# Kernel optimization log

Measured on AMD Instinct MI355X. Metric: run time of the kernel, lower is better.

The kernel has to match this reference:

```python
import jax, jax.numpy as jnp
import numpy as np

N_NODES = 50000
N_EDGES = 800000
IN_CH = 128
HID = 64
HEADS = 4
OUT_CH = 32
NEG_SLOPE = 0.2


def _glorot(key, shape):
    fan = shape[0] + shape[-1]
    return jax.random.normal(key, shape, dtype=jnp.float32) * jnp.sqrt(2.0 / fan)


def setup_inputs() -> dict:
    key = jax.random.key(0)
    ks = jax.random.split(key, 10)
    x = jax.random.normal(ks[0], (N_NODES, IN_CH), dtype=jnp.float32)
    edge_index = jax.random.randint(ks[1], (2, N_EDGES), 0, N_NODES, dtype=jnp.int32)
    # Layer 1: in -> HEADS*HID, concat=True
    W1 = _glorot(ks[2], (IN_CH, HEADS * HID))
    att_src1 = _glorot(ks[3], (HEADS, HID))
    att_dst1 = _glorot(ks[4], (HEADS, HID))
    b1 = jnp.zeros((HEADS * HID,), dtype=jnp.float32)
    # Layer 2: HEADS*HID -> OUT_CH, heads=1, concat=False
    W2 = _glorot(ks[5], (HEADS * HID, OUT_CH))
    att_src2 = _glorot(ks[6], (1, OUT_CH))
    att_dst2 = _glorot(ks[7], (1, OUT_CH))
    b2 = jnp.zeros((OUT_CH,), dtype=jnp.float32)
    return {"x": x, "edge_index": edge_index, "W1": W1, "att_src1": att_src1,
            "att_dst1": att_dst1, "b1": b1, "W2": W2, "att_src2": att_src2,
            "att_dst2": att_dst2, "b2": b2}


def _segment_softmax(logits, seg, num_segments):
    # logits: [E, H], softmax over edges sharing the same target node
    m = jax.ops.segment_max(logits, seg, num_segments=num_segments)  # [N, H]
    ex = jnp.exp(logits - m[seg])
    s = jax.ops.segment_sum(ex, seg, num_segments=num_segments)
    return ex / (s[seg] + 1e-16)


def _gat_layer(x, edge_index, W, att_src, att_dst, bias, heads, concat):
    N = x.shape[0]
    C = att_src.shape[-1]
    h = (x @ W).reshape(N, heads, C)                 # [N, H, C]
    a_src = jnp.sum(h * att_src, axis=-1)            # [N, H]
    a_dst = jnp.sum(h * att_dst, axis=-1)            # [N, H]
    src, dst = edge_index[0], edge_index[1]
    logits = jax.nn.leaky_relu(a_src[src] + a_dst[dst], NEG_SLOPE)  # [E, H]
    alpha = _segment_softmax(logits, dst, N)         # [E, H]
    msg = h[src] * alpha[:, :, None]                 # [E, H, C]
    out = jax.ops.segment_sum(msg, dst, num_segments=N)  # [N, H, C]
    out = out.reshape(N, heads * C) if concat else out.mean(axis=1)
    return out + bias


def reference(x, edge_index, W1, att_src1, att_dst1, b1, W2, att_src2, att_dst2, b2):
    # dropout omitted (eval mode)
    h = _gat_layer(x, edge_index, W1, att_src1, att_dst1, b1, HEADS, True)
    h = jax.nn.elu(h)
    out = _gat_layer(h, edge_index, W2, att_src2, att_dst2, b2, 1, False)
    return out
```

## Files before the change

kernel.cpp:

```cpp
#include <hip/hip_runtime.h>
#include <hip/hip_bf16.h>
#include <hip/hip_fp16.h>

#define NEG_SLOPE 0.2f

typedef _Float16 half8 __attribute__((ext_vector_type(8)));
typedef float f32x4 __attribute__((ext_vector_type(4)));

__device__ __forceinline__ float lrelu(float x) { return x >= 0.f ? x : NEG_SLOPE * x; }

__device__ __forceinline__ float4 h4_to_f4(float2 r) {
    __half2 a = *(__half2*)&r.x;
    __half2 b = *(__half2*)&r.y;
    float2 fa = __half22float2(a), fb = __half22float2(b);
    return make_float4(fa.x, fa.y, fb.x, fb.y);
}

__device__ __forceinline__ void fma4(float a, float4 v, float4& acc) {
    acc.x = fmaf(a, v.x, acc.x); acc.y = fmaf(a, v.y, acc.y);
    acc.z = fmaf(a, v.z, acc.z); acc.w = fmaf(a, v.w, acc.w);
}


__global__ void k_hist(const int* __restrict__ dst, int* __restrict__ counts, int E) {
    int e = blockIdx.x * 256 + threadIdx.x;
    if (e < E) atomicAdd(&counts[dst[e]], 1);
}

__global__ __launch_bounds__(256) void k_scan1(const int* __restrict__ counts,
                                               int* __restrict__ bsum, int N) {
    __shared__ int wsum[4];
    int b = blockIdx.x, t = threadIdx.x;
    int i0 = b * 1024 + t * 4;
    int s = 0;
    if (i0 < N) { int4 v = *(const int4*)&counts[i0]; s = v.x + v.y + v.z + v.w; }
#pragma unroll
    for (int off = 32; off; off >>= 1) s += __shfl_down(s, off);
    if ((t & 63) == 0) wsum[t >> 6] = s;
    __syncthreads();
    if (t == 0) bsum[b] = wsum[0] + wsum[1] + wsum[2] + wsum[3];
}

__global__ void k_scan2(const int* __restrict__ bsum, int* __restrict__ boff,
                        int* __restrict__ row_ptrN, int nb) {
    int t = threadIdx.x;
    int v = (t < nb) ? bsum[t] : 0;
    int incl = v;
#pragma unroll
    for (int off = 1; off < 64; off <<= 1) {
        int u = __shfl_up(incl, off);
        if (t >= off) incl += u;
    }
    if (t < nb) boff[t] = incl - v;
    if (t == nb - 1) *row_ptrN = incl;
}

__global__ __launch_bounds__(256) void k_scan3(const int* __restrict__ counts,
                                               const int* __restrict__ boff,
                                               int* __restrict__ row_ptr,
                                               int* __restrict__ row_fill, int N) {
    __shared__ int lds[256];
    int b = blockIdx.x, t = threadIdx.x;
    int i0 = b * 1024 + t * 4;
    int4 v = make_int4(0, 0, 0, 0);
    if (i0 < N) v = *(const int4*)&counts[i0];
    int tot = v.x + v.y + v.z + v.w;
    lds[t] = tot;
    __syncthreads();
    for (int off = 1; off < 256; off <<= 1) {
        int u = (t >= off) ? lds[t - off] : 0;
        __syncthreads();
        lds[t] += u;
        __syncthreads();
    }
    int excl = lds[t] - tot;
    int run = boff[b] + excl;
    if (i0 < N) {
        row_ptr[i0] = run;     row_fill[i0] = run;     run += v.x;
        row_ptr[i0 + 1] = run; row_fill[i0 + 1] = run; run += v.y;
        row_ptr[i0 + 2] = run; row_fill[i0 + 2] = run; run += v.z;
        row_ptr[i0 + 3] = run; row_fill[i0 + 3] = run;
    }
}

__global__ void k_scatter(const int* __restrict__ src, const int* __restrict__ dst,
                          int* __restrict__ row_fill, int* __restrict__ esrc, int E) {
    int e = blockIdx.x * 256 + threadIdx.x;
    if (e < E) {
        int p = atomicAdd(&row_fill[dst[e]], 1);
        esrc[p] = src[e];
    }
}


__global__ __launch_bounds__(128) void k_w1t(const float* __restrict__ W,
                                             __half* __restrict__ Wt) {
    int n = blockIdx.x;
    int k = threadIdx.x;
    Wt[n * 128 + k] = __float2half(W[(size_t)k * 256 + n]);
}


__global__ __launch_bounds__(256, 3) void k_gemm1(const float* __restrict__ x,
                                                  const __half* __restrict__ Wt,
                                                  const float* __restrict__ att_src,
                                                  const float* __restrict__ att_dst,
                                                  __half* __restrict__ h,
                                                  float* __restrict__ a_s,
                                                  float* __restrict__ a_d, int M) {
    __shared__ __align__(16) __half Xs[64 * 128];
    __shared__ __align__(16) __half Ws[128 * 128];
    const int tid = threadIdx.x;
    const int row0 = blockIdx.x * 64;
    const int by = blockIdx.y;
    const int col0 = by * 128;

    for (int t = 0; t < 4; ++t) {
        int c = tid + t * 256;
        int row = c >> 4, ch = c & 15;
        int r = row0 + row;
        float4 va = make_float4(0.f, 0.f, 0.f, 0.f), vb = va;
        if (r < M) {
            va = *(const float4*)&x[(size_t)r * 128 + ch * 8];
            vb = *(const float4*)&x[(size_t)r * 128 + ch * 8 + 4];
        }
        half8 hv;
        hv[0] = (_Float16)va.x; hv[1] = (_Float16)va.y;
        hv[2] = (_Float16)va.z; hv[3] = (_Float16)va.w;
        hv[4] = (_Float16)vb.x; hv[5] = (_Float16)vb.y;
        hv[6] = (_Float16)vb.z; hv[7] = (_Float16)vb.w;
        *(half8*)((char*)Xs + row * 256 + ((ch * 16) ^ ((row & 7) << 4))) = hv;
    }
    for (int t = 0; t < 8; ++t) {
        int c = tid + t * 256;
        int n = c >> 4, ch = c & 15;
        float4 v = *(const float4*)&Wt[(size_t)(col0 + n) * 128 + ch * 8];
        *(float4*)((char*)Ws + n * 256 + ((ch * 16) ^ ((n & 7) << 4))) = v;
    }
    __syncthreads();

    const int w = tid >> 6, lane = tid & 63;
    const int col_l = lane & 15, kgrp = lane >> 4;
    const int arow = w * 16 + col_l;
    const int sw = (col_l & 7) << 4;

    f32x4 acc[8];
#pragma unroll
    for (int nt = 0; nt < 8; ++nt) acc[nt] = (f32x4){0.f, 0.f, 0.f, 0.f};

#pragma unroll
    for (int ks = 0; ks < 4; ++ks) {
        int kchunk = (ks * 4 + kgrp) * 16;
        half8 av = *(const half8*)((const char*)Xs + arow * 256 + (kchunk ^ sw));
#pragma unroll
        for (int nt = 0; nt < 8; ++nt) {
            half8 bv = *(const half8*)((const char*)Ws + (nt * 16 + col_l) * 256 + (kchunk ^ sw));
            acc[nt] = __builtin_amdgcn_mfma_f32_16x16x32_f16(av, bv, acc[nt], 0, 0, 0);
        }
    }

    float asv[8], adv[8];
#pragma unroll
    for (int nt = 0; nt < 8; ++nt) {
        int gc = col0 + nt * 16 + col_l;
        asv[nt] = att_src[gc];
        adv[nt] = att_dst[gc];
    }
    const int rbase = row0 + w * 16 + kgrp * 4;
#pragma unroll
    for (int reg = 0; reg < 4; ++reg) {
        int gr = rbase + reg;
        if (gr < M) {
#pragma unroll
            for (int nt = 0; nt < 8; ++nt)
                h[(size_t)gr * 256 + col0 + nt * 16 + col_l] = __float2half(acc[nt][reg]);
        }
        float s0 = 0.f, d0 = 0.f, s1 = 0.f, d1 = 0.f;
#pragma unroll
        for (int nt = 0; nt < 4; ++nt) {
            s0 = fmaf(acc[nt][reg], asv[nt], s0);
            d0 = fmaf(acc[nt][reg], adv[nt], d0);
            s1 = fmaf(acc[nt + 4][reg], asv[nt + 4], s1);
            d1 = fmaf(acc[nt + 4][reg], adv[nt + 4], d1);
        }
#pragma unroll
        for (int off = 1; off < 16; off <<= 1) {
            s0 += __shfl_xor(s0, off); d0 += __shfl_xor(d0, off);
            s1 += __shfl_xor(s1, off); d1 += __shfl_xor(d1, off);
        }
        if (col_l == 0 && gr < M) {
            a_s[(size_t)gr * 4 + by * 2]     = s0;
            a_s[(size_t)gr * 4 + by * 2 + 1] = s1;
            a_d[(size_t)gr * 4 + by * 2]     = d0;
            a_d[(size_t)gr * 4 + by * 2 + 1] = d1;
        }
    }
}


__global__ __launch_bounds__(256) void k_alpha1(const float* __restrict__ asrc,
                                                const float* __restrict__ adst,
                                                const int* __restrict__ row_ptr,
                                                const int* __restrict__ esrc,
                                                float* __restrict__ alpha, int N) {
    int wv = threadIdx.x >> 6, lane = threadIdx.x & 63;
    int n = blockIdx.x * 4 + wv;
    if (n >= N) return;
    int e0 = row_ptr[n], e1 = row_ptr[n + 1];
    int deg = e1 - e0;
    if (deg == 0) return;
    const float4 ad = *(const float4*)&adst[(size_t)n * 4];
    if (deg <= 64) {
        float4 l = make_float4(-3e38f, -3e38f, -3e38f, -3e38f);
        if (lane < deg) {
            int s = esrc[e0 + lane];
            float4 as = *(const float4*)&asrc[(size_t)s * 4];
            l.x = lrelu(as.x + ad.x); l.y = lrelu(as.y + ad.y);
            l.z = lrelu(as.z + ad.z); l.w = lrelu(as.w + ad.w);
        }
        float4 m = l;
#pragma unroll
        for (int off = 32; off; off >>= 1) {
            m.x = fmaxf(m.x, __shfl_xor(m.x, off));
            m.y = fmaxf(m.y, __shfl_xor(m.y, off));
            m.z = fmaxf(m.z, __shfl_xor(m.z, off));
            m.w = fmaxf(m.w, __shfl_xor(m.w, off));
        }
        if (lane < deg) {
            float4 p;
            p.x = __expf(l.x - m.x); p.y = __expf(l.y - m.y);
            p.z = __expf(l.z - m.z); p.w = __expf(l.w - m.w);
            *(float4*)&alpha[(size_t)(e0 + lane) * 4] = p;
        }
    } else {
        float4 m = make_float4(-3e38f, -3e38f, -3e38f, -3e38f);
        for (int p0 = e0; p0 < e1; p0 += 64) {
            int e = p0 + lane;
            if (e < e1) {
                int s = esrc[e];
                float4 as = *(const float4*)&asrc[(size_t)s * 4];
                m.x = fmaxf(m.x, lrelu(as.x + ad.x));
                m.y = fmaxf(m.y, lrelu(as.y + ad.y));
                m.z = fmaxf(m.z, lrelu(as.z + ad.z));
                m.w = fmaxf(m.w, lrelu(as.w + ad.w));
            }
        }
#pragma unroll
        for (int off = 32; off; off >>= 1) {
            m.x = fmaxf(m.x, __shfl_xor(m.x, off));
            m.y = fmaxf(m.y, __shfl_xor(m.y, off));
            m.z = fmaxf(m.z, __shfl_xor(m.z, off));
            m.w = fmaxf(m.w, __shfl_xor(m.w, off));
        }
        for (int p0 = e0; p0 < e1; p0 += 64) {
            int e = p0 + lane;
            if (e < e1) {
                int s = esrc[e];
                float4 as = *(const float4*)&asrc[(size_t)s * 4];
                float4 p;
                p.x = __expf(lrelu(as.x + ad.x) - m.x);
                p.y = __expf(lrelu(as.y + ad.y) - m.y);
                p.z = __expf(lrelu(as.z + ad.z) - m.z);
                p.w = __expf(lrelu(as.w + ad.w) - m.w);
                *(float4*)&alpha[(size_t)e * 4] = p;
            }
        }
    }
}


__global__ __launch_bounds__(256) void k_agg1(const __half* __restrict__ h1,
                                              const int* __restrict__ row_ptr,
                                              const int* __restrict__ esrc,
                                              const float* __restrict__ alpha,
                                              const float* __restrict__ b1,
                                              float* __restrict__ y1, int N) {
    __shared__ int ss[4][64];
    __shared__ float sa[4][64 * 4];
    int tid = threadIdx.x;
    int wv = tid >> 6, lane = tid & 63;
    int n = blockIdx.x * 4 + wv;
    if (n >= N) return;
    int head = lane >> 4;
    int e0 = row_ptr[n], e1 = row_ptr[n + 1];
    float4 acc = make_float4(0.f, 0.f, 0.f, 0.f);
    float4 asum = make_float4(0.f, 0.f, 0.f, 0.f);

    for (int p0 = e0; p0 < e1; p0 += 64) {
        int cnt = min(64, e1 - p0);
        if (lane < cnt) {
            ss[wv][lane] = esrc[p0 + lane];
            float4 a4 = *(const float4*)&alpha[(size_t)(p0 + lane) * 4];
            *(float4*)&sa[wv][lane * 4] = a4;
            asum.x += a4.x; asum.y += a4.y; asum.z += a4.z; asum.w += a4.w;
        }
        int i = 0;
        for (; i + 3 < cnt; i += 4) {
            int s0 = ss[wv][i], s1 = ss[wv][i + 1], s2 = ss[wv][i + 2], s3 = ss[wv][i + 3];
            float a0 = sa[wv][i * 4 + head],       a1 = sa[wv][(i + 1) * 4 + head];
            float a2 = sa[wv][(i + 2) * 4 + head], a3 = sa[wv][(i + 3) * 4 + head];
            float2 r0 = *(const float2*)&h1[(size_t)s0 * 256 + lane * 4];
            float2 r1 = *(const float2*)&h1[(size_t)s1 * 256 + lane * 4];
            float2 r2 = *(const float2*)&h1[(size_t)s2 * 256 + lane * 4];
            float2 r3 = *(const float2*)&h1[(size_t)s3 * 256 + lane * 4];
            fma4(a0, h4_to_f4(r0), acc);
            fma4(a1, h4_to_f4(r1), acc);
            fma4(a2, h4_to_f4(r2), acc);
            fma4(a3, h4_to_f4(r3), acc);
        }
        for (; i < cnt; ++i) {
            int s0 = ss[wv][i];
            float a0 = sa[wv][i * 4 + head];
            float2 r0 = *(const float2*)&h1[(size_t)s0 * 256 + lane * 4];
            fma4(a0, h4_to_f4(r0), acc);
        }
    }

#pragma unroll
    for (int off = 1; off < 64; off <<= 1) {
        asum.x += __shfl_xor(asum.x, off);
        asum.y += __shfl_xor(asum.y, off);
        asum.z += __shfl_xor(asum.z, off);
        asum.w += __shfl_xor(asum.w, off);
    }
    float ssum = (head == 0) ? asum.x : (head == 1) ? asum.y : (head == 2) ? asum.z : asum.w;
    float inv = 1.f / (ssum + 1e-16f);
    float4 bb = *(const float4*)&b1[lane * 4];
    float4 v;
    v.x = acc.x * inv + bb.x; v.y = acc.y * inv + bb.y;
    v.z = acc.z * inv + bb.z; v.w = acc.w * inv + bb.w;
    v.x = (v.x > 0.f) ? v.x : (__expf(v.x) - 1.f);
    v.y = (v.y > 0.f) ? v.y : (__expf(v.y) - 1.f);
    v.z = (v.z > 0.f) ? v.z : (__expf(v.z) - 1.f);
    v.w = (v.w > 0.f) ? v.w : (__expf(v.w) - 1.f);
    *(float4*)&y1[(size_t)n * 256 + lane * 4] = v;
}


__global__ __launch_bounds__(256) void k_gemm2(const float* __restrict__ y1,
                                               const float* __restrict__ W,
                                               const float* __restrict__ att_src,
                                               const float* __restrict__ att_dst,
                                               __half* __restrict__ h2,
                                               float* __restrict__ a_s,
                                               float* __restrict__ a_d, int M) {
    __shared__ float xs[256][32];
    __shared__ float ws2[256 * 32];
    int tid = threadIdx.x;
    int row0 = blockIdx.x * 32;
    for (int t = tid; t < 2048; t += 256) {
        int k4 = t >> 5, m = t & 31;
        int r = row0 + m;
        float4 v = make_float4(0.f, 0.f, 0.f, 0.f);
        if (r < M) v = *(const float4*)&y1[(size_t)r * 256 + k4 * 4];
        xs[k4 * 4 + 0][m] = v.x;
        xs[k4 * 4 + 1][m] = v.y;
        xs[k4 * 4 + 2][m] = v.z;
        xs[k4 * 4 + 3][m] = v.w;
    }
    for (int t = tid; t < 2048; t += 256)
        *(float4*)&ws2[t * 4] = *(const float4*)&W[t * 4];
    __syncthreads();

    int tx = tid & 7, ty = tid >> 3;
    float acc[4] = {};
#pragma unroll 4
    for (int k = 0; k < 256; ++k) {
        float a = xs[k][ty];
        float4 b = *(const float4*)&ws2[k * 32 + tx * 4];
        acc[0] += a * b.x; acc[1] += a * b.y; acc[2] += a * b.z; acc[3] += a * b.w;
    }
    int r = row0 + ty;
    if (r < M) {
        __half2 p01 = __floats2half2_rn(acc[0], acc[1]);
        __half2 p23 = __floats2half2_rn(acc[2], acc[3]);
        float2 st;
        *(__half2*)&st.x = p01;
        *(__half2*)&st.y = p23;
        *(float2*)&h2[(size_t)r * 32 + tx * 4] = st;
    }

    float s_ = 0.f, d_ = 0.f;
#pragma unroll
    for (int j = 0; j < 4; ++j) {
        s_ = fmaf(acc[j], att_src[tx * 4 + j], s_);
        d_ = fmaf(acc[j], att_dst[tx * 4 + j], d_);
    }
#pragma unroll
    for (int off = 1; off < 8; off <<= 1) {
        s_ += __shfl_xor(s_, off);
        d_ += __shfl_xor(d_, off);
    }
    if (tx == 0 && r < M) { a_s[r] = s_; a_d[r] = d_; }
}


__global__ __launch_bounds__(256) void k_alpha2(const float* __restrict__ asrc,
                                                const float* __restrict__ adst,
                                                const int* __restrict__ row_ptr,
                                                const int* __restrict__ esrc,
                                                float* __restrict__ alpha, int N) {
    int g = threadIdx.x >> 5, c = threadIdx.x & 31;
    int n = blockIdx.x * 8 + g;
    if (n >= N) return;
    int e0 = row_ptr[n], e1 = row_ptr[n + 1];
    int deg = e1 - e0;
    if (deg == 0) return;
    float ad = adst[n];
    if (deg <= 32) {
        float l = -3e38f;
        if (c < deg) l = lrelu(asrc[esrc[e0 + c]] + ad);
        float m = l;
#pragma unroll
        for (int off = 16; off; off >>= 1) m = fmaxf(m, __shfl_xor(m, off, 32));
        if (c < deg) alpha[e0 + c] = __expf(l - m);
    } else {
        float m = -3e38f;
        for (int p0 = e0; p0 < e1; p0 += 32) {
            int e = p0 + c;
            if (e < e1) m = fmaxf(m, lrelu(asrc[esrc[e]] + ad));
        }
#pragma unroll
        for (int off = 16; off; off >>= 1) m = fmaxf(m, __shfl_xor(m, off, 32));
        for (int p0 = e0; p0 < e1; p0 += 32) {
            int e = p0 + c;
            if (e < e1) alpha[e] = __expf(lrelu(asrc[esrc[e]] + ad) - m);
        }
    }
}


__global__ __launch_bounds__(256) void k_agg2(const __half* __restrict__ h2,
                                              const int* __restrict__ row_ptr,
                                              const int* __restrict__ esrc,
                                              const float* __restrict__ alpha,
                                              const float* __restrict__ b2,
                                              float* __restrict__ out, int N) {
    __shared__ int ss[4][64];
    __shared__ float sa[4][64];
    int tid = threadIdx.x;
    int wv = tid >> 6, lane = tid & 63;
    int n = blockIdx.x * 4 + wv;
    if (n >= N) return;
    int grp = lane >> 4, cl = lane & 15;
    int e0 = row_ptr[n], e1 = row_ptr[n + 1];
    float2 acc = make_float2(0.f, 0.f);
    float asum = 0.f;

    for (int p0 = e0; p0 < e1; p0 += 64) {
        int cnt = min(64, e1 - p0);
        if (lane < cnt) {
            ss[wv][lane] = esrc[p0 + lane];
            float a = alpha[p0 + lane];
            sa[wv][lane] = a;
            asum += a;
        }
        int i = 0;
        for (; i + 7 < cnt; i += 8) {
            int ea = i + grp, eb = i + 4 + grp;
            int s0 = ss[wv][ea], s1 = ss[wv][eb];
            float a0 = sa[wv][ea], a1 = sa[wv][eb];
            __half2 v0 = *(const __half2*)&h2[(size_t)s0 * 32 + cl * 2];
            __half2 v1 = *(const __half2*)&h2[(size_t)s1 * 32 + cl * 2];
            float2 f0 = __half22float2(v0), f1 = __half22float2(v1);
            acc.x = fmaf(a0, f0.x, acc.x); acc.y = fmaf(a0, f0.y, acc.y);
            acc.x = fmaf(a1, f1.x, acc.x); acc.y = fmaf(a1, f1.y, acc.y);
        }
        for (; i < cnt; i += 4) {
            int e = i + grp;
            if (e < cnt) {
                int s0 = ss[wv][e];
                float a0 = sa[wv][e];
                __half2 v0 = *(const __half2*)&h2[(size_t)s0 * 32 + cl * 2];
                float2 f0 = __half22float2(v0);
                acc.x = fmaf(a0, f0.x, acc.x); acc.y = fmaf(a0, f0.y, acc.y);
            }
        }
    }
    acc.x += __shfl_xor(acc.x, 16); acc.y += __shfl_xor(acc.y, 16);
    acc.x += __shfl_xor(acc.x, 32); acc.y += __shfl_xor(acc.y, 32);
#pragma unroll
    for (int off = 1; off < 64; off <<= 1) asum += __shfl_xor(asum, off);
    if (grp == 0) {
        float inv = 1.f / (asum + 1e-16f);
        float2 o;
        o.x = acc.x * inv + b2[cl * 2];
        o.y = acc.y * inv + b2[cl * 2 + 1];
        *(float2*)&out[(size_t)n * 32 + cl * 2] = o;
    }
}


extern "C" void kernel_launch(void* const* d_in, const int* in_sizes, int n_in,
                              void* d_out, int out_size, void* d_ws, size_t ws_size,
                              hipStream_t stream) {
    const float* x   = (const float*)d_in[0];
    const int*   ei  = (const int*)d_in[1];
    const float* W1  = (const float*)d_in[2];
    const float* as1 = (const float*)d_in[3];
    const float* ad1 = (const float*)d_in[4];
    const float* b1  = (const float*)d_in[5];
    const float* W2  = (const float*)d_in[6];
    const float* as2 = (const float*)d_in[7];
    const float* ad2 = (const float*)d_in[8];
    const float* b2  = (const float*)d_in[9];
    float* out = (float*)d_out;

    const int N = in_sizes[0] / 128;
    const int E = in_sizes[1] / 2;
    const int* src = ei;
    const int* dstp = ei + E;
    const int nb = (N + 1023) / 1024;

    char* ws = (char*)d_ws;
    size_t off = 0;
    auto alloc = [&](size_t nbytes) {
        void* p = ws + off;
        off += (nbytes + 255) & ~(size_t)255;
        return p;
    };
    int* counts    = (int*)alloc((size_t)N * 4);
    int* row_ptr   = (int*)alloc((size_t)(N + 1) * 4);
    int* row_fill  = (int*)alloc((size_t)N * 4);
    int* esrc      = (int*)alloc((size_t)E * 4);
    __half* h1     = (__half*)alloc((size_t)N * 256 * 2);
    float* y1      = (float*)alloc((size_t)N * 256 * 4);
    __half* h2     = (__half*)alloc((size_t)N * 32 * 2);
    float* a_s1    = (float*)alloc((size_t)N * 4 * 4);
    float* a_d1    = (float*)alloc((size_t)N * 4 * 4);
    float* a_s2    = (float*)alloc((size_t)N * 4);
    float* a_d2    = (float*)alloc((size_t)N * 4);
    float* alpha1  = (float*)alloc((size_t)E * 4 * 4);
    float* alpha2  = (float*)alloc((size_t)E * 4);
    int* bsum      = (int*)alloc((size_t)nb * 4);
    int* boff      = (int*)alloc((size_t)nb * 4);
    __half* Wt     = (__half*)alloc((size_t)256 * 128 * 2);

    hipMemsetAsync(counts, 0, (size_t)N * 4, stream);
    k_hist<<<(E + 255) / 256, 256, 0, stream>>>(dstp, counts, E);
    k_scan1<<<nb, 256, 0, stream>>>(counts, bsum, N);
    k_scan2<<<1, 64, 0, stream>>>(bsum, boff, &row_ptr[N], nb);
    k_scan3<<<nb, 256, 0, stream>>>(counts, boff, row_ptr, row_fill, N);
    k_scatter<<<(E + 255) / 256, 256, 0, stream>>>(src, dstp, row_fill, esrc, E);

    k_w1t<<<256, 128, 0, stream>>>(W1, Wt);
    k_gemm1<<<dim3((N + 63) / 64, 2), 256, 0, stream>>>(x, Wt, as1, ad1, h1, a_s1, a_d1, N);
    k_alpha1<<<(N + 3) / 4, 256, 0, stream>>>(a_s1, a_d1, row_ptr, esrc, alpha1, N);
    k_agg1<<<(N + 3) / 4, 256, 0, stream>>>(h1, row_ptr, esrc, alpha1, b1, y1, N);

    k_gemm2<<<(N + 31) / 32, 256, 0, stream>>>(y1, W2, as2, ad2, h2, a_s2, a_d2, N);
    k_alpha2<<<(N + 7) / 8, 256, 0, stream>>>(a_s2, a_d2, row_ptr, esrc, alpha2, N);
    k_agg2<<<(N + 3) / 4, 256, 0, stream>>>(h2, row_ptr, esrc, alpha2, b2, out, N);
}
```

Measured before the change: 267.2 us.

## Fuse edge-softmax into aggregation kernels and run layer-2 GEMM on fp16 MFMA

```diff
diff --git a/kernel.cpp b/kernel.cpp
--- a/kernel.cpp
+++ b/kernel.cpp
@@ -100,6 +100,13 @@
     Wt[n * 128 + k] = __float2half(W[(size_t)k * 256 + n]);
 }
 
+__global__ __launch_bounds__(256) void k_w2t(const float* __restrict__ W,
+                                             __half* __restrict__ Wt) {
+    int n = blockIdx.x;
+    int k = threadIdx.x;
+    Wt[n * 256 + k] = __float2half(W[(size_t)k * 32 + n]);
+}
+
 
 __global__ __launch_bounds__(256, 3) void k_gemm1(const float* __restrict__ x,
                                                   const __half* __restrict__ Wt,
@@ -198,39 +205,69 @@
 }
 
 
-__global__ __launch_bounds__(256) void k_alpha1(const float* __restrict__ asrc,
-                                                const float* __restrict__ adst,
-                                                const int* __restrict__ row_ptr,
-                                                const int* __restrict__ esrc,
-                                                float* __restrict__ alpha, int N) {
-    int wv = threadIdx.x >> 6, lane = threadIdx.x & 63;
+__global__ __launch_bounds__(256) void k_agg1(const __half* __restrict__ h1,
+                                              const int* __restrict__ row_ptr,
+                                              const int* __restrict__ esrc,
+                                              const float* __restrict__ asrc,
+                                              const float* __restrict__ adst,
+                                              const float* __restrict__ b1,
+                                              __half* __restrict__ y1, int N) {
+    __shared__ int ss[4][64];
+    __shared__ float sa[4][64 * 4];
+    int tid = threadIdx.x;
+    int wv = tid >> 6, lane = tid & 63;
     int n = blockIdx.x * 4 + wv;
     if (n >= N) return;
+    int head = lane >> 4;
     int e0 = row_ptr[n], e1 = row_ptr[n + 1];
     int deg = e1 - e0;
-    if (deg == 0) return;
     const float4 ad = *(const float4*)&adst[(size_t)n * 4];
+    float4 acc = make_float4(0.f, 0.f, 0.f, 0.f);
+    float4 asum = make_float4(0.f, 0.f, 0.f, 0.f);
+
     if (deg <= 64) {
         float4 l = make_float4(-3e38f, -3e38f, -3e38f, -3e38f);
         if (lane < deg) {
             int s = esrc[e0 + lane];
+            ss[wv][lane] = s;
             float4 as = *(const float4*)&asrc[(size_t)s * 4];
             l.x = lrelu(as.x + ad.x); l.y = lrelu(as.y + ad.y);
             l.z = lrelu(as.z + ad.z); l.w = lrelu(as.w + ad.w);
         }
         float4 m = l;
 #pragma unroll
-        for (int off = 32; off; off >>= 1) {
+        for (int off = 1; off < 64; off <<= 1) {
             m.x = fmaxf(m.x, __shfl_xor(m.x, off));
             m.y = fmaxf(m.y, __shfl_xor(m.y, off));
             m.z = fmaxf(m.z, __shfl_xor(m.z, off));
             m.w = fmaxf(m.w, __shfl_xor(m.w, off));
         }
+        float4 a = make_float4(0.f, 0.f, 0.f, 0.f);
         if (lane < deg) {
-            float4 p;
-            p.x = __expf(l.x - m.x); p.y = __expf(l.y - m.y);
-            p.z = __expf(l.z - m.z); p.w = __expf(l.w - m.w);
-            *(float4*)&alpha[(size_t)(e0 + lane) * 4] = p;
+            a.x = __expf(l.x - m.x); a.y = __expf(l.y - m.y);
+            a.z = __expf(l.z - m.z); a.w = __expf(l.w - m.w);
+            *(float4*)&sa[wv][lane * 4] = a;
+        }
+        asum = a;
+        int i = 0;
+        for (; i + 3 < deg; i += 4) {
+            int s0 = ss[wv][i], s1 = ss[wv][i + 1], s2 = ss[wv][i + 2], s3 = ss[wv][i + 3];
+            float a0 = sa[wv][i * 4 + head],       a1 = sa[wv][(i + 1) * 4 + head];
+            float a2 = sa[wv][(i + 2) * 4 + head], a3 = sa[wv][(i + 3) * 4 + head];
+            float2 r0 = *(const float2*)&h1[(size_t)s0 * 256 + lane * 4];
+            float2 r1 = *(const float2*)&h1[(size_t)s1 * 256 + lane * 4];
+            float2 r2 = *(const float2*)&h1[(size_t)s2 * 256 + lane * 4];
+            float2 r3 = *(const float2*)&h1[(size_t)s3 * 256 + lane * 4];
+            fma4(a0, h4_to_f4(r0), acc);
+            fma4(a1, h4_to_f4(r1), acc);
+            fma4(a2, h4_to_f4(r2), acc);
+            fma4(a3, h4_to_f4(r3), acc);
+        }
+        for (; i < deg; ++i) {
+            int s0 = ss[wv][i];
+            float a0 = sa[wv][i * 4 + head];
+            float2 r0 = *(const float2*)&h1[(size_t)s0 * 256 + lane * 4];
+            fma4(a0, h4_to_f4(r0), acc);
         }
     } else {
         float4 m = make_float4(-3e38f, -3e38f, -3e38f, -3e38f);
@@ -246,73 +283,46 @@
             }
         }
 #pragma unroll
-        for (int off = 32; off; off >>= 1) {
+        for (int off = 1; off < 64; off <<= 1) {
             m.x = fmaxf(m.x, __shfl_xor(m.x, off));
             m.y = fmaxf(m.y, __shfl_xor(m.y, off));
             m.z = fmaxf(m.z, __shfl_xor(m.z, off));
             m.w = fmaxf(m.w, __shfl_xor(m.w, off));
         }
         for (int p0 = e0; p0 < e1; p0 += 64) {
-            int e = p0 + lane;
-            if (e < e1) {
-                int s = esrc[e];
+            int cnt = min(64, e1 - p0);
+            if (lane < cnt) {
+                int s = esrc[p0 + lane];
+                ss[wv][lane] = s;
                 float4 as = *(const float4*)&asrc[(size_t)s * 4];
-                float4 p;
-                p.x = __expf(lrelu(as.x + ad.x) - m.x);
-                p.y = __expf(lrelu(as.y + ad.y) - m.y);
-                p.z = __expf(lrelu(as.z + ad.z) - m.z);
-                p.w = __expf(lrelu(as.w + ad.w) - m.w);
-                *(float4*)&alpha[(size_t)e * 4] = p;
+                float4 a;
+                a.x = __expf(lrelu(as.x + ad.x) - m.x);
+                a.y = __expf(lrelu(as.y + ad.y) - m.y);
+                a.z = __expf(lrelu(as.z + ad.z) - m.z);
+                a.w = __expf(lrelu(as.w + ad.w) - m.w);
+                *(float4*)&sa[wv][lane * 4] = a;
+                asum.x += a.x; asum.y += a.y; asum.z += a.z; asum.w += a.w;
             }
-        }
-    }
-}
-
-
-__global__ __launch_bounds__(256) void k_agg1(const __half* __restrict__ h1,
-                                              const int* __restrict__ row_ptr,
-                                              const int* __restrict__ esrc,
-                                              const float* __restrict__ alpha,
-                                              const float* __restrict__ b1,
-                                              float* __restrict__ y1, int N) {
-    __shared__ int ss[4][64];
-    __shared__ float sa[4][64 * 4];
-    int tid = threadIdx.x;
-    int wv = tid >> 6, lane = tid & 63;
-    int n = blockIdx.x * 4 + wv;
-    if (n >= N) return;
-    int head = lane >> 4;
-    int e0 = row_ptr[n], e1 = row_ptr[n + 1];
-    float4 acc = make_float4(0.f, 0.f, 0.f, 0.f);
-    float4 asum = make_float4(0.f, 0.f, 0.f, 0.f);
-
-    for (int p0 = e0; p0 < e1; p0 += 64) {
-        int cnt = min(64, e1 - p0);
-        if (lane < cnt) {
-            ss[wv][lane] = esrc[p0 + lane];
-            float4 a4 = *(const float4*)&alpha[(size_t)(p0 + lane) * 4];
-            *(float4*)&sa[wv][lane * 4] = a4;
-            asum.x += a4.x; asum.y += a4.y; asum.z += a4.z; asum.w += a4.w;
-        }
-        int i = 0;
-        for (; i + 3 < cnt; i += 4) {
-            int s0 = ss[wv][i], s1 = ss[wv][i + 1], s2 = ss[wv][i + 2], s3 = ss[wv][i + 3];
-            float a0 = sa[wv][i * 4 + head],       a1 = sa[wv][(i + 1) * 4 + head];
-            float a2 = sa[wv][(i + 2) * 4 + head], a3 = sa[wv][(i + 3) * 4 + head];
-            float2 r0 = *(const float2*)&h1[(size_t)s0 * 256 + lane * 4];
-            float2 r1 = *(const float2*)&h1[(size_t)s1 * 256 + lane * 4];
-            float2 r2 = *(const float2*)&h1[(size_t)s2 * 256 + lane * 4];
-            float2 r3 = *(const float2*)&h1[(size_t)s3 * 256 + lane * 4];
-            fma4(a0, h4_to_f4(r0), acc);
-            fma4(a1, h4_to_f4(r1), acc);
-            fma4(a2, h4_to_f4(r2), acc);
-            fma4(a3, h4_to_f4(r3), acc);
-        }
-        for (; i < cnt; ++i) {
-            int s0 = ss[wv][i];
-            float a0 = sa[wv][i * 4 + head];
-            float2 r0 = *(const float2*)&h1[(size_t)s0 * 256 + lane * 4];
-            fma4(a0, h4_to_f4(r0), acc);
+            int i = 0;
+            for (; i + 3 < cnt; i += 4) {
+                int s0 = ss[wv][i], s1 = ss[wv][i + 1], s2 = ss[wv][i + 2], s3 = ss[wv][i + 3];
+                float a0 = sa[wv][i * 4 + head],       a1 = sa[wv][(i + 1) * 4 + head];
+                float a2 = sa[wv][(i + 2) * 4 + head], a3 = sa[wv][(i + 3) * 4 + head];
+                float2 r0 = *(const float2*)&h1[(size_t)s0 * 256 + lane * 4];
+                float2 r1 = *(const float2*)&h1[(size_t)s1 * 256 + lane * 4];
+                float2 r2 = *(const float2*)&h1[(size_t)s2 * 256 + lane * 4];
+                float2 r3 = *(const float2*)&h1[(size_t)s3 * 256 + lane * 4];
+                fma4(a0, h4_to_f4(r0), acc);
+                fma4(a1, h4_to_f4(r1), acc);
+                fma4(a2, h4_to_f4(r2), acc);
+                fma4(a3, h4_to_f4(r3), acc);
+            }
+            for (; i < cnt; ++i) {
+                int s0 = ss[wv][i];
+                float a0 = sa[wv][i * 4 + head];
+                float2 r0 = *(const float2*)&h1[(size_t)s0 * 256 + lane * 4];
+                fma4(a0, h4_to_f4(r0), acc);
+            }
         }
     }
 
@@ -333,99 +343,85 @@
     v.y = (v.y > 0.f) ? v.y : (__expf(v.y) - 1.f);
     v.z = (v.z > 0.f) ? v.z : (__expf(v.z) - 1.f);
     v.w = (v.w > 0.f) ? v.w : (__expf(v.w) - 1.f);
-    *(float4*)&y1[(size_t)n * 256 + lane * 4] = v;
-}
-
-
-__global__ __launch_bounds__(256) void k_gemm2(const float* __restrict__ y1,
-                                               const float* __restrict__ W,
-                                               const float* __restrict__ att_src,
-                                               const float* __restrict__ att_dst,
-                                               __half* __restrict__ h2,
-                                               float* __restrict__ a_s,
-                                               float* __restrict__ a_d, int M) {
-    __shared__ float xs[256][32];
-    __shared__ float ws2[256 * 32];
-    int tid = threadIdx.x;
-    int row0 = blockIdx.x * 32;
-    for (int t = tid; t < 2048; t += 256) {
-        int k4 = t >> 5, m = t & 31;
-        int r = row0 + m;
+    __half2 h01 = __floats2half2_rn(v.x, v.y);
+    __half2 h23 = __floats2half2_rn(v.z, v.w);
+    float2 st;
+    *(__half2*)&st.x = h01;
+    *(__half2*)&st.y = h23;
+    *(float2*)&y1[(size_t)n * 256 + lane * 4] = st;
+}
+
+
+__global__ __launch_bounds__(256, 3) void k_gemm2(const __half* __restrict__ y1,
+                                                  const __half* __restrict__ W2t,
+                                                  const float* __restrict__ att_src,
+                                                  const float* __restrict__ att_dst,
+                                                  __half* __restrict__ h2,
+                                                  float* __restrict__ a_s,
+                                                  float* __restrict__ a_d, int M) {
+    __shared__ __align__(16) __half Ys[64 * 256];
+    __shared__ __align__(16) __half Ws[32 * 256];
+    const int tid = threadIdx.x;
+    const int row0 = blockIdx.x * 64;
+
+    for (int t = 0; t < 8; ++t) {
+        int c = tid + t * 256;
+        int row = c >> 5, ch = c & 31;
+        int r = row0 + row;
         float4 v = make_float4(0.f, 0.f, 0.f, 0.f);
-        if (r < M) v = *(const float4*)&y1[(size_t)r * 256 + k4 * 4];
-        xs[k4 * 4 + 0][m] = v.x;
-        xs[k4 * 4 + 1][m] = v.y;
-        xs[k4 * 4 + 2][m] = v.z;
-        xs[k4 * 4 + 3][m] = v.w;
-    }
-    for (int t = tid; t < 2048; t += 256)
-        *(float4*)&ws2[t * 4] = *(const float4*)&W[t * 4];
+        if (r < M) v = *(const float4*)&y1[(size_t)r * 256 + ch * 8];
+        *(float4*)((char*)Ys + row * 512 + ((ch * 16) ^ ((row & 7) << 4))) = v;
+    }
+    for (int t = 0; t < 4; ++t) {
+        int c = tid + t * 256;
+        int n = c >> 5, ch = c & 31;
+        float4 v = *(const float4*)&W2t[(size_t)n * 256 + ch * 8];
+        *(float4*)((char*)Ws + n * 512 + ((ch * 16) ^ ((n & 7) << 4))) = v;
+    }
     __syncthreads();
 
-    int tx = tid & 7, ty = tid >> 3;
-    float acc[4] = {};
-#pragma unroll 4
-    for (int k = 0; k < 256; ++k) {
-        float a = xs[k][ty];
-        float4 b = *(const float4*)&ws2[k * 32 + tx * 4];
-        acc[0] += a * b.x; acc[1] += a * b.y; acc[2] += a * b.z; acc[3] += a * b.w;
-    }
-    int r = row0 + ty;
-    if (r < M) {
-        __half2 p01 = __floats2half2_rn(acc[0], acc[1]);
-        __half2 p23 = __floats2half2_rn(acc[2], acc[3]);
-        float2 st;
-        *(__half2*)&st.x = p01;
-        *(__half2*)&st.y = p23;
-        *(float2*)&h2[(size_t)r * 32 + tx * 4] = st;
-    }
-
-    float s_ = 0.f, d_ = 0.f;
-#pragma unroll
-    for (int j = 0; j < 4; ++j) {
-        s_ = fmaf(acc[j], att_src[tx * 4 + j], s_);
-        d_ = fmaf(acc[j], att_dst[tx * 4 + j], d_);
-    }
-#pragma unroll
-    for (int off = 1; off < 8; off <<= 1) {
-        s_ += __shfl_xor(s_, off);
-        d_ += __shfl_xor(d_, off);
-    }
-    if (tx == 0 && r < M) { a_s[r] = s_; a_d[r] = d_; }
-}
-
-
-__global__ __launch_bounds__(256) void k_alpha2(const float* __restrict__ asrc,
-                                                const float* __restrict__ adst,
-                                                const int* __restrict__ row_ptr,
-                                                const int* __restrict__ esrc,
-                                                float* __restrict__ alpha, int N) {
-    int g = threadIdx.x >> 5, c = threadIdx.x & 31;
-    int n = blockIdx.x * 8 + g;
-    if (n >= N) return;
-    int e0 = row_ptr[n], e1 = row_ptr[n + 1];
-    int deg = e1 - e0;
-    if (deg == 0) return;
-    float ad = adst[n];
-    if (deg <= 32) {
-        float l = -3e38f;
-        if (c < deg) l = lrelu(asrc[esrc[e0 + c]] + ad);
-        float m = l;
-#pragma unroll
-        for (int off = 16; off; off >>= 1) m = fmaxf(m, __shfl_xor(m, off, 32));
-        if (c < deg) alpha[e0 + c] = __expf(l - m);
-    } else {
-        float m = -3e38f;
-        for (int p0 = e0; p0 < e1; p0 += 32) {
-            int e = p0 + c;
-            if (e < e1) m = fmaxf(m, lrelu(asrc[esrc[e]] + ad));
-        }
-#pragma unroll
-        for (int off = 16; off; off >>= 1) m = fmaxf(m, __shfl_xor(m, off, 32));
-        for (int p0 = e0; p0 < e1; p0 += 32) {
-            int e = p0 + c;
-            if (e < e1) alpha[e] = __expf(lrelu(asrc[esrc[e]] + ad) - m);
-        }
+    const int w = tid >> 6, lane = tid & 63;
+    const int col_l = lane & 15, kgrp = lane >> 4;
+    const int arow = w * 16 + col_l;
+    const int sw = (col_l & 7) << 4;
+
+    f32x4 acc[2];
+    acc[0] = (f32x4){0.f, 0.f, 0.f, 0.f};
+    acc[1] = (f32x4){0.f, 0.f, 0.f, 0.f};
+
+#pragma unroll
+    for (int ks = 0; ks < 8; ++ks) {
+        int kchunk = (ks * 4 + kgrp) * 16;
+        half8 av = *(const half8*)((const char*)Ys + arow * 512 + (kchunk ^ sw));
+#pragma unroll
+        for (int nt = 0; nt < 2; ++nt) {
+            half8 bv = *(const half8*)((const char*)Ws + (nt * 16 + col_l) * 512 + (kchunk ^ sw));
+            acc[nt] = __builtin_amdgcn_mfma_f32_16x16x32_f16(av, bv, acc[nt], 0, 0, 0);
+        }
+    }
+
+    float asv[2], adv[2];
+#pragma unroll
+    for (int nt = 0; nt < 2; ++nt) {
+        asv[nt] = att_src[nt * 16 + col_l];
+        adv[nt] = att_dst[nt * 16 + col_l];
+    }
+    const int rbase = row0 + w * 16 + kgrp * 4;
+#pragma unroll
+    for (int reg = 0; reg < 4; ++reg) {
+        int gr = rbase + reg;
+        if (gr < M) {
+            h2[(size_t)gr * 32 + col_l]      = __float2half(acc[0][reg]);
+            h2[(size_t)gr * 32 + 16 + col_l] = __float2half(acc[1][reg]);
+        }
+        float s_ = fmaf(acc[0][reg], asv[0], acc[1][reg] * asv[1]);
+        float d_ = fmaf(acc[0][reg], adv[0], acc[1][reg] * adv[1]);
+#pragma unroll
+        for (int off = 1; off < 16; off <<= 1) {
+            s_ += __shfl_xor(s_, off);
+            d_ += __shfl_xor(d_, off);
+        }
+        if (col_l == 0 && gr < M) { a_s[gr] = s_; a_d[gr] = d_; }
     }
 }
 
@@ -433,7 +429,8 @@
 __global__ __launch_bounds__(256) void k_agg2(const __half* __restrict__ h2,
                                               const int* __restrict__ row_ptr,
                                               const int* __restrict__ esrc,
-                                              const float* __restrict__ alpha,
+                                              const float* __restrict__ asrc,
+                                              const float* __restrict__ adst,
                                               const float* __restrict__ b2,
                                               float* __restrict__ out, int N) {
     __shared__ int ss[4][64];
@@ -444,17 +441,12 @@
     if (n >= N) return;
     int grp = lane >> 4, cl = lane & 15;
     int e0 = row_ptr[n], e1 = row_ptr[n + 1];
+    int deg = e1 - e0;
+    float ad = adst[n];
     float2 acc = make_float2(0.f, 0.f);
     float asum = 0.f;
 
-    for (int p0 = e0; p0 < e1; p0 += 64) {
-        int cnt = min(64, e1 - p0);
-        if (lane < cnt) {
-            ss[wv][lane] = esrc[p0 + lane];
-            float a = alpha[p0 + lane];
-            sa[wv][lane] = a;
-            asum += a;
-        }
+    auto gather = [&](int cnt) {
         int i = 0;
         for (; i + 7 < cnt; i += 8) {
             int ea = i + grp, eb = i + 4 + grp;
@@ -476,7 +468,46 @@
                 acc.x = fmaf(a0, f0.x, acc.x); acc.y = fmaf(a0, f0.y, acc.y);
             }
         }
-    }
+    };
+
+    if (deg <= 64) {
+        float l = -3e38f;
+        if (lane < deg) {
+            int s = esrc[e0 + lane];
+            ss[wv][lane] = s;
+            l = lrelu(asrc[s] + ad);
+        }
+        float m = l;
+#pragma unroll
+        for (int off = 1; off < 64; off <<= 1) m = fmaxf(m, __shfl_xor(m, off));
+        float a = 0.f;
+        if (lane < deg) {
+            a = __expf(l - m);
+            sa[wv][lane] = a;
+        }
+        asum = a;
+        gather(deg);
+    } else {
+        float m = -3e38f;
+        for (int p0 = e0; p0 < e1; p0 += 64) {
+            int e = p0 + lane;
+            if (e < e1) m = fmaxf(m, lrelu(asrc[esrc[e]] + ad));
+        }
+#pragma unroll
+        for (int off = 1; off < 64; off <<= 1) m = fmaxf(m, __shfl_xor(m, off));
+        for (int p0 = e0; p0 < e1; p0 += 64) {
+            int cnt = min(64, e1 - p0);
+            if (lane < cnt) {
+                int s = esrc[p0 + lane];
+                ss[wv][lane] = s;
+                float a = __expf(lrelu(asrc[s] + ad) - m);
+                sa[wv][lane] = a;
+                asum += a;
+            }
+            gather(cnt);
+        }
+    }
+
     acc.x += __shfl_xor(acc.x, 16); acc.y += __shfl_xor(acc.y, 16);
     acc.x += __shfl_xor(acc.x, 32); acc.y += __shfl_xor(acc.y, 32);
 #pragma unroll
@@ -524,17 +555,16 @@
     int* row_fill  = (int*)alloc((size_t)N * 4);
     int* esrc      = (int*)alloc((size_t)E * 4);
     __half* h1     = (__half*)alloc((size_t)N * 256 * 2);
-    float* y1      = (float*)alloc((size_t)N * 256 * 4);
+    __half* y1     = (__half*)alloc((size_t)N * 256 * 2);
     __half* h2     = (__half*)alloc((size_t)N * 32 * 2);
     float* a_s1    = (float*)alloc((size_t)N * 4 * 4);
     float* a_d1    = (float*)alloc((size_t)N * 4 * 4);
     float* a_s2    = (float*)alloc((size_t)N * 4);
     float* a_d2    = (float*)alloc((size_t)N * 4);
-    float* alpha1  = (float*)alloc((size_t)E * 4 * 4);
-    float* alpha2  = (float*)alloc((size_t)E * 4);
     int* bsum      = (int*)alloc((size_t)nb * 4);
     int* boff      = (int*)alloc((size_t)nb * 4);
     __half* Wt     = (__half*)alloc((size_t)256 * 128 * 2);
+    __half* W2t    = (__half*)alloc((size_t)32 * 256 * 2);
 
     hipMemsetAsync(counts, 0, (size_t)N * 4, stream);
     k_hist<<<(E + 255) / 256, 256, 0, stream>>>(dstp, counts, E);
@@ -544,11 +574,11 @@
     k_scatter<<<(E + 255) / 256, 256, 0, stream>>>(src, dstp, row_fill, esrc, E);
 
     k_w1t<<<256, 128, 0, stream>>>(W1, Wt);
+    k_w2t<<<32, 256, 0, stream>>>(W2, W2t);
+
     k_gemm1<<<dim3((N + 63) / 64, 2), 256, 0, stream>>>(x, Wt, as1, ad1, h1, a_s1, a_d1, N);
-    k_alpha1<<<(N + 3) / 4, 256, 0, stream>>>(a_s1, a_d1, row_ptr, esrc, alpha1, N);
-    k_agg1<<<(N + 3) / 4, 256, 0, stream>>>(h1, row_ptr, esrc, alpha1, b1, y1, N);
-
-    k_gemm2<<<(N + 31) / 32, 256, 0, stream>>>(y1, W2, as2, ad2, h2, a_s2, a_d2, N);
-    k_alpha2<<<(N + 7) / 8, 256, 0, stream>>>(a_s2, a_d2, row_ptr, esrc, alpha2, N);
-    k_agg2<<<(N + 3) / 4, 256, 0, stream>>>(h2, row_ptr, esrc, alpha2, b2, out, N);
-}
+    k_agg1<<<(N + 3) / 4, 256, 0, stream>>>(h1, row_ptr, esrc, a_s1, a_d1, b1, y1, N);
+
+    k_gemm2<<<(N + 63) / 64, 256, 0, stream>>>(y1, W2t, as2, ad2, h2, a_s2, a_d2, N);
+    k_agg2<<<(N + 3) / 4, 256, 0, stream>>>(h2, row_ptr, esrc, a_s2, a_d2, b2, out, N);
+}
```

After: 220.6 us. -17.5%, faster.
